# Optimization experiments

Hardware: AMD Instinct MI355X
Metric: run time of the kernel (lower is better)

Reference implementation:

```python
import jax, jax.numpy as jnp
import numpy as np

B, L, D, H = 4, 2048, 1024, 16
DK = D // H
SCALE = 1.0 / (DK ** 0.5)


def setup_inputs() -> dict:
    key = jax.random.key(0)
    ks = jax.random.split(key, 7)
    std = 1.0 / np.sqrt(D)
    return {
        "q": jax.random.normal(ks[0], (B, L, D), jnp.float32),
        "k": jax.random.normal(ks[1], (B, L, D), jnp.float32),
        "v": jax.random.normal(ks[2], (B, L, D), jnp.float32),
        # torch nn.Linear weights: shape (out_features, in_features)
        "w_q": jax.random.normal(ks[3], (D, D), jnp.float32) * std,
        "w_k": jax.random.normal(ks[4], (D, D), jnp.float32) * std,
        "w_v": jax.random.normal(ks[5], (D, D), jnp.float32) * std,
        "w_o": jax.random.normal(ks[6], (D, D), jnp.float32) * std,
    }


def _split_heads(x):
    # (B, L, D) -> (B, H, L, DK)
    return x.reshape(B, L, H, DK).transpose(0, 2, 1, 3)


def reference(q, k, v, w_q, w_k, w_v, w_o):
    # Linear projections (no bias): y = x @ W^T
    qh = _split_heads(jnp.einsum('bld,ed->ble', q, w_q))
    kh = _split_heads(jnp.einsum('bld,ed->ble', k, w_k))
    vh = _split_heads(jnp.einsum('bld,ed->ble', v, w_v))
    # scaled dot-product attention; score is (B, H, L, L)
    score = jnp.einsum('bhqd,bhkd->bhqk', qh, kh) * SCALE
    probs = jax.nn.softmax(score, axis=-1)  # dropout p=0.0 -> identity
    attn = jnp.einsum('bhqk,bhkd->bhqd', probs, vh)
    # merge heads and output projection
    o = attn.transpose(0, 2, 1, 3).reshape(B, L, D)
    return jnp.einsum('bld,ed->ble', o, w_o)
```

## Files before the change

kernel.cpp:

```cpp
#include <hip/hip_runtime.h>
#include <stdint.h>

typedef unsigned short u16;
typedef __attribute__((ext_vector_type(8))) short short8;
typedef __attribute__((ext_vector_type(4))) float floatx4;

#define DEV __device__ __forceinline__

DEV u16 f2bf(float f) {
  union { float f; unsigned u; } x; x.f = f;
  unsigned u = x.u + 0x7fffu + ((x.u >> 16) & 1u);
  return (u16)(u >> 16);
}
DEV float scrub(float x) {
  return fminf(fmaxf(x, -65504.0f), 65504.0f);
}
DEV void async16(const void* g, void* l) {
  auto gp = reinterpret_cast<const __attribute__((address_space(1))) unsigned int*>(
      reinterpret_cast<uintptr_t>(g));
  auto lp = reinterpret_cast<__attribute__((address_space(3))) unsigned int*>(
      reinterpret_cast<uintptr_t>(l));
  __builtin_amdgcn_global_load_lds(gp, lp, 16, 0, 0);
}
DEV unsigned asu(float f) { union { float f; unsigned u; } x; x.f = f; return x.u; }
DEV float asf(unsigned u) { union { unsigned u; float f; } x; x.u = u; return x.f; }

__global__ void cvt7(const float* __restrict__ a, const float* __restrict__ b,
                     const float* __restrict__ c, const float* __restrict__ w0,
                     const float* __restrict__ w1, const float* __restrict__ w2,
                     const float* __restrict__ w3,
                     u16* __restrict__ oa, u16* __restrict__ ob, u16* __restrict__ oc,
                     u16* __restrict__ o0, u16* __restrict__ o1, u16* __restrict__ o2,
                     u16* __restrict__ o3,
                     int n4a, int n4w) {
  int z = blockIdx.z;
  const float* s;
  u16* d;
  int n4;
  switch (z) {
    case 0: s = a;  d = oa; n4 = n4a; break;
    case 1: s = b;  d = ob; n4 = n4a; break;
    case 2: s = c;  d = oc; n4 = n4a; break;
    case 3: s = w0; d = o0; n4 = n4w; break;
    case 4: s = w1; d = o1; n4 = n4w; break;
    case 5: s = w2; d = o2; n4 = n4w; break;
    default: s = w3; d = o3; n4 = n4w; break;
  }
  int i = blockIdx.x * 256 + threadIdx.x;
  if (i < n4) {
    float4 v = ((const float4*)s)[i];
    union { u16 h[4]; uint2 u; } o;
    o.h[0] = f2bf(v.x); o.h[1] = f2bf(v.y); o.h[2] = f2bf(v.z); o.h[3] = f2bf(v.w);
    ((uint2*)d)[i] = o.u;
  }
}

__global__ __launch_bounds__(256, 2) void proj3(
    const u16* __restrict__ Xq, const u16* __restrict__ Xk, const u16* __restrict__ Xv,
    const u16* __restrict__ Wq, const u16* __restrict__ Wk, const u16* __restrict__ Wv,
    u16* __restrict__ Oq, u16* __restrict__ Ok, u16* __restrict__ Ov)
{
  constexpr int K = 1024;
  constexpr float SC2 = 0.125f * 1.44269504088896f;
  int flat = blockIdx.x + 8 * (blockIdx.y + 64 * blockIdx.z);
  int swz = (flat & 7) * 192 + (flat >> 3);
  const int bx = swz & 7, by = (swz >> 3) & 63, z = swz >> 9;

  const u16* X = z == 0 ? Xq : (z == 1 ? Xk : Xv);
  const u16* W = z == 0 ? Wq : (z == 1 ? Wk : Wv);
  u16* Out = z == 0 ? Oq : (z == 1 ? Ok : Ov);

  const u16* A = (z < 2) ? W : X;
  const u16* Bp = (z < 2) ? X : W;
  const int m0 = (z < 2) ? bx * 128 : by * 128;
  const int n0 = (z < 2) ? by * 128 : bx * 128;

  const int tid = threadIdx.x;
  const int w = tid >> 6, lane = tid & 63;
  const int quad = lane >> 4, l16 = lane & 15;
  const int wm = (w & 1) * 64, wn = (w >> 1) * 64;

  __shared__ u16 As[128 * 64];
  __shared__ u16 Bs[128 * 64];

  floatx4 acc[4][4];
#pragma unroll
  for (int i = 0; i < 4; ++i)
#pragma unroll
    for (int j = 0; j < 4; ++j) acc[i][j] = (floatx4)0.0f;

  for (int k0 = 0; k0 < K; k0 += 64) {
#pragma unroll
    for (int i = 0; i < 4; ++i) {
      int lin = i * 256 + tid;
      int r = lin >> 3, sp = lin & 7, s = sp ^ (r & 7);
      async16(A + (size_t)(m0 + r) * K + k0 + s * 8, &As[lin * 8]);
    }
#pragma unroll
    for (int i = 0; i < 4; ++i) {
      int lin = i * 256 + tid;
      int r = lin >> 3, sp = lin & 7, s = sp ^ (r & 7);
      async16(Bp + (size_t)(n0 + r) * K + k0 + s * 8, &Bs[lin * 8]);
    }
    asm volatile("s_waitcnt vmcnt(0)" ::: "memory");
    __syncthreads();

#pragma unroll
    for (int kk = 0; kk < 2; ++kk) {
      short8 af[4], bf[4];
#pragma unroll
      for (int mi = 0; mi < 4; ++mi) {
        int r = wm + mi * 16 + l16;
        af[mi] = *(const short8*)&As[r * 64 + (((kk * 4 + quad) ^ (r & 7)) * 8)];
      }
#pragma unroll
      for (int ni = 0; ni < 4; ++ni) {
        int r = wn + ni * 16 + l16;
        bf[ni] = *(const short8*)&Bs[r * 64 + (((kk * 4 + quad) ^ (r & 7)) * 8)];
      }
#pragma unroll
      for (int mi = 0; mi < 4; ++mi)
#pragma unroll
        for (int ni = 0; ni < 4; ++ni)
          acc[mi][ni] = __builtin_amdgcn_mfma_f32_16x16x32_bf16(af[mi], bf[ni], acc[mi][ni], 0, 0, 0);
    }
    __syncthreads();
  }

  const float sc = (z == 0) ? SC2 : 1.0f;
#pragma unroll
  for (int mi = 0; mi < 4; ++mi) {
#pragma unroll
    for (int ni = 0; ni < 4; ++ni) {
      int rr = m0 + wm + mi * 16 + quad * 4;
      int cc = n0 + wn + ni * 16 + l16;
      u16 h0 = f2bf(sc * acc[mi][ni][0]);
      u16 h1 = f2bf(sc * acc[mi][ni][1]);
      u16 h2 = f2bf(sc * acc[mi][ni][2]);
      u16 h3 = f2bf(sc * acc[mi][ni][3]);
      uint2 dw; dw.x = h0 | ((unsigned)h1 << 16); dw.y = h2 | ((unsigned)h3 << 16);
      if (z < 2) {
        int bb = cc >> 11, ll = cc & 2047;
        int hh = rr >> 6, dk0 = rr & 63;
        *(uint2*)&Out[(((size_t)bb * 16 + hh) * 2048 + ll) * 64 + dk0] = dw;
      } else {
        int bb = rr >> 11, ll0 = rr & 2047;
        int hh = cc >> 6, dk = cc & 63;
        *(uint2*)&Out[(((size_t)bb * 16 + hh) * 64 + dk) * 2048 + ll0] = dw;
      }
    }
  }
}

__global__ __launch_bounds__(256, 2) void gemm_out(
    const u16* __restrict__ Ah, const u16* __restrict__ Wo, float* __restrict__ Out)
{
  constexpr int K = 1024;
  const int tid = threadIdx.x;
  const int w = tid >> 6, lane = tid & 63;
  const int quad = lane >> 4, l16 = lane & 15;
  int flat = blockIdx.x + 8 * blockIdx.y;
  int swz = (flat & 7) * 64 + (flat >> 3);
  const int bx = swz & 7, by = swz >> 3;
  const int m0 = by * 128, n0 = bx * 128;
  const int wm = (w & 1) * 64, wn = (w >> 1) * 64;

  __shared__ u16 As[128 * 64];
  __shared__ u16 Bs[128 * 64];

  floatx4 acc[4][4];
#pragma unroll
  for (int i = 0; i < 4; ++i)
#pragma unroll
    for (int j = 0; j < 4; ++j) acc[i][j] = (floatx4)0.0f;

  for (int k0 = 0; k0 < K; k0 += 64) {
#pragma unroll
    for (int i = 0; i < 4; ++i) {
      int lin = i * 256 + tid;
      int r = lin >> 3, sp = lin & 7, s = sp ^ (r & 7);
      int row = m0 + r;
      const u16* ga = Ah + (((size_t)(row >> 11) * 16 + (k0 >> 6)) * 2048 + (row & 2047)) * 64 + s * 8;
      async16(ga, &As[lin * 8]);
    }
#pragma unroll
    for (int i = 0; i < 4; ++i) {
      int lin = i * 256 + tid;
      int r = lin >> 3, sp = lin & 7, s = sp ^ (r & 7);
      async16(Wo + (size_t)(n0 + r) * K + k0 + s * 8, &Bs[lin * 8]);
    }
    asm volatile("s_waitcnt vmcnt(0)" ::: "memory");
    __syncthreads();

#pragma unroll
    for (int kk = 0; kk < 2; ++kk) {
      short8 af[4], bf[4];
#pragma unroll
      for (int mi = 0; mi < 4; ++mi) {
        int r = wm + mi * 16 + l16;
        af[mi] = *(const short8*)&As[r * 64 + (((kk * 4 + quad) ^ (r & 7)) * 8)];
      }
#pragma unroll
      for (int ni = 0; ni < 4; ++ni) {
        int r = wn + ni * 16 + l16;
        bf[ni] = *(const short8*)&Bs[r * 64 + (((kk * 4 + quad) ^ (r & 7)) * 8)];
      }
#pragma unroll
      for (int mi = 0; mi < 4; ++mi)
#pragma unroll
        for (int ni = 0; ni < 4; ++ni)
          acc[mi][ni] = __builtin_amdgcn_mfma_f32_16x16x32_bf16(af[mi], bf[ni], acc[mi][ni], 0, 0, 0);
    }
    __syncthreads();
  }

#pragma unroll
  for (int mi = 0; mi < 4; ++mi)
#pragma unroll
    for (int ni = 0; ni < 4; ++ni) {
      int rr = m0 + wm + mi * 16 + quad * 4;
      int cc = n0 + wn + ni * 16 + l16;
#pragma unroll
      for (int reg = 0; reg < 4; ++reg)
        Out[(size_t)(rr + reg) * 1024 + cc] = scrub(acc[mi][ni][reg]);
    }
}

__global__ __launch_bounds__(256, 4) void attn3(
    const u16* Qh, const u16* __restrict__ Kh,
    const u16* __restrict__ VT, u16* O)
{
  constexpr int L = 2048, DK = 64, H = 16;
  const int tid = threadIdx.x;
  const int w = tid >> 6, lane = tid & 63;
  const int quad = lane >> 4, l16 = lane & 15;
  int flat = blockIdx.x + 16 * (blockIdx.y + 16 * blockIdx.z);
  int swz = (flat & 7) * 128 + (flat >> 3);
  const int q0 = (swz & 15) * 128;
  const int bh = swz >> 4;

  __shared__ u16 SM[4 * 64 * 64];
  u16* const QP = &SM[8192];
  char* const SMb = (char*)&SM[0];

  const u16* Qg = Qh + ((size_t)bh * L + q0) * DK;
  const u16* Kb = Kh + (size_t)bh * L * DK;
  const u16* Vb = VT + (size_t)bh * DK * L;

#pragma unroll
  for (int i = 0; i < 4; ++i) {
    int lin = i * 256 + tid;
    int r = lin >> 3, sp = lin & 7, s = sp ^ (r & 7);
    async16(Qg + (size_t)r * DK + s * 8, &QP[lin * 8]);
  }

  const int rA = tid >> 3;
  const int sA = (tid & 7) ^ (rA & 7);
  const u16* kg0 = Kb + (size_t)rA * DK + sA * 8;
  const u16* kg1 = kg0 + 32 * DK;
  const u16* vg0 = Vb + (size_t)rA * L + sA * 8;
  const u16* vg1 = vg0 + (size_t)32 * L;
  u16* const ldsB0 = &SM[tid * 8];
  u16* const ldsB1 = &SM[8192 + tid * 8];

  async16(kg0, ldsB0);
  async16(kg1, ldsB0 + 2048);
  async16(vg0, ldsB0 + 4096);
  async16(vg1, ldsB0 + 6144);
  kg0 += 64 * DK; kg1 += 64 * DK; vg0 += 64; vg1 += 64;

  asm volatile("s_waitcnt vmcnt(0)" ::: "memory");
  __syncthreads();

  short8 qf[2][2];
#pragma unroll
  for (int mi = 0; mi < 2; ++mi)
#pragma unroll
    for (int kk = 0; kk < 2; ++kk) {
      int r = w * 32 + mi * 16 + l16;
      qf[mi][kk] = *(const short8*)&QP[r * 64 + (((kk * 4 + quad) ^ (r & 7)) * 8)];
    }
  asm volatile("s_waitcnt lgkmcnt(0)" ::: "memory");
  __syncthreads();

  const int l7 = l16 & 7, qh2 = quad >> 1, qo = (quad & 1) * 8;
  int ka[2], vo[4];
#pragma unroll
  for (int kk = 0; kk < 2; ++kk)
    ka[kk] = l16 * 128 + (((kk * 4 + quad) ^ l7) * 16);
#pragma unroll
  for (int j = 0; j < 4; ++j)
    vo[j] = l16 * 128 + (((qh2 + 2 * j) ^ l7) * 16) + qo;

  short8 onesv;
#pragma unroll
  for (int j = 0; j < 8; ++j) onesv[j] = (short)0x3F80;

  floatx4 oT[4][2];
  floatx4 lacc[2];
#pragma unroll
  for (int nd = 0; nd < 4; ++nd)
#pragma unroll
    for (int mi = 0; mi < 2; ++mi) oT[nd][mi] = (floatx4)0.0f;
  lacc[0] = (floatx4)0.0f;
  lacc[1] = (floatx4)0.0f;

  auto body = [&](int PB, u16* ldsN, bool more) {
    if (more) {
      async16(kg0, ldsN);
      async16(kg1, ldsN + 2048);
      async16(vg0, ldsN + 4096);
      async16(vg1, ldsN + 6144);
      kg0 += 64 * DK; kg1 += 64 * DK; vg0 += 64; vg1 += 64;
    }

    floatx4 sT[4][2];
#pragma unroll
    for (int t = 0; t < 4; ++t)
#pragma unroll
      for (int mi = 0; mi < 2; ++mi) sT[t][mi] = (floatx4)0.0f;
    __builtin_amdgcn_s_setprio(1);
#pragma unroll
    for (int kk = 0; kk < 2; ++kk)
#pragma unroll
      for (int t = 0; t < 4; ++t) {
        short8 kf = *(const short8*)(SMb + PB + t * 2048 + ka[kk]);
#pragma unroll
        for (int mi = 0; mi < 2; ++mi)
          sT[t][mi] = __builtin_amdgcn_mfma_f32_16x16x32_bf16(kf, qf[mi][kk], sT[t][mi], 0, 0, 0);
      }
    __builtin_amdgcn_s_setprio(0);

#pragma unroll
    for (int t = 0; t < 4; ++t)
#pragma unroll
      for (int mi = 0; mi < 2; ++mi)
#pragma unroll
        for (int r = 0; r < 4; ++r) sT[t][mi][r] = __builtin_amdgcn_exp2f(sT[t][mi][r]);

    short8 pf[2][2];
#pragma unroll
    for (int g = 0; g < 2; ++g)
#pragma unroll
      for (int mi = 0; mi < 2; ++mi) {
        union { unsigned u[4]; short8 v; } up;
        up.u[0] = __builtin_amdgcn_perm(asu(sT[2 * g][mi][1]), asu(sT[2 * g][mi][0]), 0x07060302u);
        up.u[1] = __builtin_amdgcn_perm(asu(sT[2 * g][mi][3]), asu(sT[2 * g][mi][2]), 0x07060302u);
        up.u[2] = __builtin_amdgcn_perm(asu(sT[2 * g + 1][mi][1]), asu(sT[2 * g + 1][mi][0]), 0x07060302u);
        up.u[3] = __builtin_amdgcn_perm(asu(sT[2 * g + 1][mi][3]), asu(sT[2 * g + 1][mi][2]), 0x07060302u);
        pf[g][mi] = up.v;
      }

    __builtin_amdgcn_s_setprio(1);
#pragma unroll
    for (int g = 0; g < 2; ++g) {
#pragma unroll
      for (int nd = 0; nd < 4; ++nd) {
        union { uint2 ab[2]; short8 v; } uv;
        uv.ab[0] = *(const uint2*)(SMb + PB + 8192 + nd * 2048 + vo[2 * g]);
        uv.ab[1] = *(const uint2*)(SMb + PB + 8192 + nd * 2048 + vo[2 * g + 1]);
#pragma unroll
        for (int mi = 0; mi < 2; ++mi)
          oT[nd][mi] = __builtin_amdgcn_mfma_f32_16x16x32_bf16(uv.v, pf[g][mi], oT[nd][mi], 0, 0, 0);
      }
#pragma unroll
      for (int mi = 0; mi < 2; ++mi)
        lacc[mi] = __builtin_amdgcn_mfma_f32_16x16x32_bf16(onesv, pf[g][mi], lacc[mi], 0, 0, 0);
    }
    __builtin_amdgcn_s_setprio(0);

    asm volatile("s_waitcnt vmcnt(0)" ::: "memory");
    __syncthreads();
  };

  for (int j0 = 0; j0 < L; j0 += 128) {
    asm volatile("" : "+v"(ka[0]), "+v"(ka[1]),
                      "+v"(vo[0]), "+v"(vo[1]), "+v"(vo[2]), "+v"(vo[3]));
    body(0, ldsB1, true);
    body(16384, ldsB0, j0 + 128 < L);
  }

#pragma unroll
  for (int mi = 0; mi < 2; ++mi) {
    float inv = 1.0f / fmaxf(lacc[mi][0], 1e-30f);
    int token = q0 + w * 32 + mi * 16 + l16;
#pragma unroll
    for (int nd = 0; nd < 4; ++nd) {
      u16 h0 = f2bf(scrub(oT[nd][mi][0] * inv));
      u16 h1 = f2bf(scrub(oT[nd][mi][1] * inv));
      u16 h2 = f2bf(scrub(oT[nd][mi][2] * inv));
      u16 h3 = f2bf(scrub(oT[nd][mi][3] * inv));
      uint2 dw; dw.x = h0 | ((unsigned)h1 << 16); dw.y = h2 | ((unsigned)h3 << 16);
      *(uint2*)&O[((size_t)bh * L + token) * 64 + nd * 16 + quad * 4] = dw;
    }
  }
}

extern "C" void kernel_launch(void* const* d_in, const int* in_sizes, int n_in,
                              void* d_out, int out_size, void* d_ws, size_t ws_size,
                              hipStream_t stream) {
  const float* q  = (const float*)d_in[0];
  const float* k  = (const float*)d_in[1];
  const float* v  = (const float*)d_in[2];
  const float* wq = (const float*)d_in[3];
  const float* wk = (const float*)d_in[4];
  const float* wv = (const float*)d_in[5];
  const float* wo = (const float*)d_in[6];
  float* out = (float*)d_out;

  const size_t NE = (size_t)4 * 16 * 2048 * 64;
  const size_t WN = (size_t)1024 * 1024;

  u16* qb  = (u16*)d_ws;
  u16* kb  = qb + NE;
  u16* vb  = kb + NE;
  u16* wqb = vb + NE;
  u16* wkb = wqb + WN;
  u16* wvb = wkb + WN;
  u16* wob = wvb + WN;
  u16* Qh  = wob + WN;
  u16* Kh  = (u16*)d_out;
  u16* VTg = Kh + NE;

  int n4a = (int)(NE / 4), n4w = (int)(WN / 4);
  cvt7<<<dim3((n4a + 255) / 256, 1, 7), 256, 0, stream>>>(
      q, k, v, wq, wk, wv, wo, qb, kb, vb, wqb, wkb, wvb, wob, n4a, n4w);

  dim3 g1(8, 64, 3);
  proj3<<<g1, dim3(256), 0, stream>>>(qb, kb, vb, wqb, wkb, wvb, Qh, Kh, VTg);

  dim3 g2(16, 16, 4);
  attn3<<<g2, dim3(256), 0, stream>>>(Qh, Kh, VTg, Qh);

  dim3 g3(8, 64, 1);
  gemm_out<<<g3, dim3(256), 0, stream>>>(Qh, wob, out);
}
```

Baseline: 313.2 us.

## Double-buffer LDS tiles in projection GEMMs to overlap loads with MFMA

Both the QKV projection GEMM and the output projection GEMM now use two LDS stages. The loads for the next K-tile are issued before computing the current one, and the wait plus barrier happen only at the end of each iteration, so global-to-LDS latency is hidden behind MFMA work. The MFMA section is also wrapped in s_setprio to favour the compute waves. LDS use doubles to 64KB per block, which may lower occupancy below the launch_bounds target of 2 blocks.

```diff
diff --git a/kernel.cpp b/kernel.cpp
--- a/kernel.cpp
+++ b/kernel.cpp
@@ -80,43 +80,52 @@
   const int quad = lane >> 4, l16 = lane & 15;
   const int wm = (w & 1) * 64, wn = (w >> 1) * 64;
 
-  __shared__ u16 As[128 * 64];
-  __shared__ u16 Bs[128 * 64];
-
-  floatx4 acc[4][4];
-#pragma unroll
-  for (int i = 0; i < 4; ++i)
-#pragma unroll
-    for (int j = 0; j < 4; ++j) acc[i][j] = (floatx4)0.0f;
-
-  for (int k0 = 0; k0 < K; k0 += 64) {
+  __shared__ u16 SM[32768];
+
+  auto stage = [&](int p, int k0) {
 #pragma unroll
     for (int i = 0; i < 4; ++i) {
       int lin = i * 256 + tid;
       int r = lin >> 3, sp = lin & 7, s = sp ^ (r & 7);
-      async16(A + (size_t)(m0 + r) * K + k0 + s * 8, &As[lin * 8]);
+      async16(A + (size_t)(m0 + r) * K + k0 + s * 8, &SM[p * 8192 + lin * 8]);
     }
 #pragma unroll
     for (int i = 0; i < 4; ++i) {
       int lin = i * 256 + tid;
       int r = lin >> 3, sp = lin & 7, s = sp ^ (r & 7);
-      async16(Bp + (size_t)(n0 + r) * K + k0 + s * 8, &Bs[lin * 8]);
-    }
-    asm volatile("s_waitcnt vmcnt(0)" ::: "memory");
-    __syncthreads();
-
+      async16(Bp + (size_t)(n0 + r) * K + k0 + s * 8, &SM[16384 + p * 8192 + lin * 8]);
+    }
+  };
+
+  floatx4 acc[4][4];
+#pragma unroll
+  for (int i = 0; i < 4; ++i)
+#pragma unroll
+    for (int j = 0; j < 4; ++j) acc[i][j] = (floatx4)0.0f;
+
+  stage(0, 0);
+  asm volatile("s_waitcnt vmcnt(0)" ::: "memory");
+  __syncthreads();
+
+  for (int k0 = 0; k0 < K; k0 += 64) {
+    const int p = (k0 >> 6) & 1;
+    if (k0 + 64 < K) stage(p ^ 1, k0 + 64);
+    const u16* Asp = &SM[p * 8192];
+    const u16* Bsp = &SM[16384 + p * 8192];
+
+    __builtin_amdgcn_s_setprio(1);
 #pragma unroll
     for (int kk = 0; kk < 2; ++kk) {
       short8 af[4], bf[4];
 #pragma unroll
       for (int mi = 0; mi < 4; ++mi) {
         int r = wm + mi * 16 + l16;
-        af[mi] = *(const short8*)&As[r * 64 + (((kk * 4 + quad) ^ (r & 7)) * 8)];
+        af[mi] = *(const short8*)&Asp[r * 64 + (((kk * 4 + quad) ^ (r & 7)) * 8)];
       }
 #pragma unroll
       for (int ni = 0; ni < 4; ++ni) {
         int r = wn + ni * 16 + l16;
-        bf[ni] = *(const short8*)&Bs[r * 64 + (((kk * 4 + quad) ^ (r & 7)) * 8)];
+        bf[ni] = *(const short8*)&Bsp[r * 64 + (((kk * 4 + quad) ^ (r & 7)) * 8)];
       }
 #pragma unroll
       for (int mi = 0; mi < 4; ++mi)
@@ -124,6 +133,9 @@
         for (int ni = 0; ni < 4; ++ni)
           acc[mi][ni] = __builtin_amdgcn_mfma_f32_16x16x32_bf16(af[mi], bf[ni], acc[mi][ni], 0, 0, 0);
     }
+    __builtin_amdgcn_s_setprio(0);
+
+    asm volatile("s_waitcnt vmcnt(0)" ::: "memory");
     __syncthreads();
   }
 
@@ -165,45 +177,54 @@
   const int m0 = by * 128, n0 = bx * 128;
   const int wm = (w & 1) * 64, wn = (w >> 1) * 64;
 
-  __shared__ u16 As[128 * 64];
-  __shared__ u16 Bs[128 * 64];
-
-  floatx4 acc[4][4];
-#pragma unroll
-  for (int i = 0; i < 4; ++i)
-#pragma unroll
-    for (int j = 0; j < 4; ++j) acc[i][j] = (floatx4)0.0f;
-
-  for (int k0 = 0; k0 < K; k0 += 64) {
+  __shared__ u16 SM[32768];
+
+  auto stage = [&](int p, int k0) {
 #pragma unroll
     for (int i = 0; i < 4; ++i) {
       int lin = i * 256 + tid;
       int r = lin >> 3, sp = lin & 7, s = sp ^ (r & 7);
       int row = m0 + r;
       const u16* ga = Ah + (((size_t)(row >> 11) * 16 + (k0 >> 6)) * 2048 + (row & 2047)) * 64 + s * 8;
-      async16(ga, &As[lin * 8]);
+      async16(ga, &SM[p * 8192 + lin * 8]);
     }
 #pragma unroll
     for (int i = 0; i < 4; ++i) {
       int lin = i * 256 + tid;
       int r = lin >> 3, sp = lin & 7, s = sp ^ (r & 7);
-      async16(Wo + (size_t)(n0 + r) * K + k0 + s * 8, &Bs[lin * 8]);
-    }
-    asm volatile("s_waitcnt vmcnt(0)" ::: "memory");
-    __syncthreads();
-
+      async16(Wo + (size_t)(n0 + r) * K + k0 + s * 8, &SM[16384 + p * 8192 + lin * 8]);
+    }
+  };
+
+  floatx4 acc[4][4];
+#pragma unroll
+  for (int i = 0; i < 4; ++i)
+#pragma unroll
+    for (int j = 0; j < 4; ++j) acc[i][j] = (floatx4)0.0f;
+
+  stage(0, 0);
+  asm volatile("s_waitcnt vmcnt(0)" ::: "memory");
+  __syncthreads();
+
+  for (int k0 = 0; k0 < K; k0 += 64) {
+    const int p = (k0 >> 6) & 1;
+    if (k0 + 64 < K) stage(p ^ 1, k0 + 64);
+    const u16* Asp = &SM[p * 8192];
+    const u16* Bsp = &SM[16384 + p * 8192];
+
+    __builtin_amdgcn_s_setprio(1);
 #pragma unroll
     for (int kk = 0; kk < 2; ++kk) {
       short8 af[4], bf[4];
 #pragma unroll
       for (int mi = 0; mi < 4; ++mi) {
         int r = wm + mi * 16 + l16;
-        af[mi] = *(const short8*)&As[r * 64 + (((kk * 4 + quad) ^ (r & 7)) * 8)];
+        af[mi] = *(const short8*)&Asp[r * 64 + (((kk * 4 + quad) ^ (r & 7)) * 8)];
       }
 #pragma unroll
       for (int ni = 0; ni < 4; ++ni) {
         int r = wn + ni * 16 + l16;
-        bf[ni] = *(const short8*)&Bs[r * 64 + (((kk * 4 + quad) ^ (r & 7)) * 8)];
+        bf[ni] = *(const short8*)&Bsp[r * 64 + (((kk * 4 + quad) ^ (r & 7)) * 8)];
       }
 #pragma unroll
       for (int mi = 0; mi < 4; ++mi)
@@ -211,6 +232,9 @@
         for (int ni = 0; ni < 4; ++ni)
           acc[mi][ni] = __builtin_amdgcn_mfma_f32_16x16x32_bf16(af[mi], bf[ni], acc[mi][ni], 0, 0, 0);
     }
+    __builtin_amdgcn_s_setprio(0);
+
+    asm volatile("s_waitcnt vmcnt(0)" ::: "memory");
     __syncthreads();
   }
 
```

Result: no change. 315.9 us (+0.9%).
